# Kernel tuning notes

Measured on AMD Instinct MI355X. Metric: run time of the kernel, lower is better.

Reference implementation:

```python
import jax, jax.numpy as jnp
import numpy as np

# per-amino-acid residue lengths (heavy atoms - 1), 20 types, sorted ascending for readability
RES_LEN_NP = np.array([3, 4, 5, 5, 6, 6, 6, 7, 7, 7, 7, 7, 8, 8, 8, 9, 10, 10, 11, 13], dtype=np.int32)
LMAX = int(RES_LEN_NP.max())  # 13
N_TYPES = 20
N_RES = 2048
BATCH = 16
DV_ATM = 64
DV_AMN = 64


def _atoms_for(seq_types_np):
    return int(RES_LEN_NP[seq_types_np].sum())


def setup_inputs() -> dict:
    key = jax.random.key(0)
    k1, k2, k3, k4 = jax.random.split(key, 4)
    seq_np = (np.arange(N_RES) % N_TYPES).astype(np.int32)
    atoms = _atoms_for(seq_np)  # 15036
    pos_atm = jax.random.normal(k1, (BATCH, atoms, 3), dtype=jnp.float32)
    pos_amn = jax.random.normal(k2, (BATCH, N_RES, 3), dtype=jnp.float32)
    scale = 1.0 / np.sqrt(LMAX)
    W_amn = jax.random.normal(k3, (N_TYPES, DV_AMN, LMAX), dtype=jnp.float32) * scale
    W_atm = jax.random.normal(k4, (N_TYPES, LMAX, DV_ATM, LMAX), dtype=jnp.float32) * scale
    return {
        "pos_atm": pos_atm,
        "pos_amn": pos_amn,
        "W_amn": W_amn,
        "W_atm": W_atm,
        "seq_types": jnp.asarray(seq_np),
    }


def reference(pos_atm, pos_amn, W_amn, W_atm, seq_types):
    """Vectorized equivalent of the per-residue loop:
    for each residue i of type t with length L_t:
      diff = pos_atm[:, start_i:start_i+L_t] - pos_amn[:, i, None]        # (B, L_t, 3)
      x_v_amn[:, i] = einsum('ol,bld->bod', W_amn[t, :, :L_t], diff)       # (B, Damn, 3)
      x_v_atm block  = einsum('mvl,bld->bmvd', W_atm[t, :L_t, :, :L_t], diff)
    Residues are padded to LMAX and batched; padding is masked out.
    """
    res_len = jnp.asarray(RES_LEN_NP)
    B, atoms, _ = pos_atm.shape
    lens = res_len[seq_types]                                  # (N,)
    starts = jnp.concatenate([jnp.zeros((1,), lens.dtype), jnp.cumsum(lens)[:-1]])
    ar = jnp.arange(LMAX, dtype=lens.dtype)
    atom_idx = jnp.clip(starts[:, None] + ar[None, :], 0, atoms - 1)  # (N, LMAX)
    mask = ar[None, :] < lens[:, None]                                 # (N, LMAX)

    # diffs: (B, N, LMAX, 3), zeroed at padding
    diffs = (pos_atm[:, atom_idx] - pos_amn[:, :, None, :]) * mask[None, :, :, None]

    Wa = W_amn[seq_types]                                      # (N, Damn, LMAX)
    x_v_amn = jnp.einsum('bnld,nol->bnod', diffs, Wa)          # (B, N, Damn, 3)

    Wt = W_atm[seq_types]                                      # (N, LMAX, Dv, LMAX)
    xa = jnp.einsum('bnld,nmvl->bnmvd', diffs, Wt)             # (B, N, LMAX, Dv, 3)
    xa = xa * mask[None, :, :, None, None]

    # scatter padded per-residue atom outputs back to the flat atom axis;
    # invalid slots go to a dummy row `atoms` that is sliced off
    idx = jnp.where(mask, atom_idx, atoms).reshape(-1)         # (N*LMAX,)
    xa_flat = xa.reshape(B, -1, DV_ATM, 3)                     # (B, N*LMAX, Dv, 3)
    x_v_atm = jnp.zeros((B, atoms + 1, DV_ATM, 3), pos_atm.dtype).at[:, idx].add(xa_flat)[:, :atoms]
    return x_v_atm, x_v_amn
```

## Files before the change

### kernel.cpp

```cpp
#include <hip/hip_runtime.h>

#define N_RES 2048
#define BATCH 16
#define LMAX  13
#define NSLOT 14
#define VPAD  68
#define DV    64

__device__ __constant__ int RES_LEN_D[20] = {3,4,5,5,6,6,6,7,7,7,7,7,8,8,8,9,10,10,11,13};

__global__ __launch_bounds__(256, 3)
void posmix_kernel(const float* __restrict__ pos_atm,
                   const float* __restrict__ pos_amn,
                   const float* __restrict__ W_amn,
                   const float* __restrict__ W_atm,
                   const int*   __restrict__ seq,
                   float* __restrict__ out_atm,
                   float* __restrict__ out_amn,
                   int atoms)
{
  const int i   = blockIdx.x;
  const int tid = threadIdx.x;
  const int t   = seq[i];
  const int L   = RES_LEN_D[t];

  __shared__ float w_lds[NSLOT * LMAX * VPAD];
  __shared__ float diff_lds[BATCH * LMAX * 4];

  int* red = (int*)w_lds;
  {
    int s = 0;
    int base = tid * 8;
    #pragma unroll
    for (int k = 0; k < 8; ++k) {
      int r = base + k;
      if (r < i) s += RES_LEN_D[seq[r]];
    }
    red[tid] = s;
  }
  __syncthreads();
  #pragma unroll
  for (int off = 128; off > 0; off >>= 1) {
    if (tid < off) red[tid] += red[tid + off];
    __syncthreads();
  }
  const int start = red[0];
  __syncthreads();

  if (tid < BATCH * LMAX) {
    int b = tid / LMAX;
    int l = tid - b * LMAX;
    float dx = 0.f, dy = 0.f, dz = 0.f;
    if (l < L) {
      const float* pa = pos_atm + ((size_t)b * atoms + (size_t)(start + l)) * 3;
      const float* pm = pos_amn + ((size_t)b * N_RES + i) * 3;
      dx = pa[0] - pm[0];
      dy = pa[1] - pm[1];
      dz = pa[2] - pm[2];
    }
    *(float4*)(diff_lds + tid * 4) = make_float4(dx, dy, dz, 0.f);
  }

  {
    const float* Wt = W_atm + (size_t)t * (LMAX * DV * LMAX);
    const int total = L * DV * LMAX;
    for (int g = tid; g < total; g += 256) {
      int m = g / (DV * LMAX);
      int r = g - m * (DV * LMAX);
      int v = r / LMAX;
      int l = r - v * LMAX;
      w_lds[(m * LMAX + l) * VPAD + v] = Wt[g];
    }
    const float* Wa = W_amn + (size_t)t * (DV * LMAX);
    for (int g = tid; g < DV * LMAX; g += 256) {
      int o = g / LMAX;
      int l = g - o * LMAX;
      w_lds[(L * LMAX + l) * VPAD + o] = Wa[g];
    }
  }
  __syncthreads();

  const int Lp1 = L + 1;
  const int ntasks = 64 * Lp1;

  for (int task = tid; task < ntasks; task += 256) {
    int vo   = task & 7;
    int rest = task >> 3;
    int bp   = rest / Lp1;
    int m    = rest - bp * Lp1;

    float acc0[24], acc1[24];
    #pragma unroll
    for (int k = 0; k < 24; ++k) { acc0[k] = 0.f; acc1[k] = 0.f; }

    const float* wr = w_lds + (m * LMAX) * VPAD + vo * 8;
    const float* dr = diff_lds + (bp * 2) * (LMAX * 4);

    for (int l = 0; l < L; ++l) {
      float4 w0 = *(const float4*)(wr + l * VPAD);
      float4 w1 = *(const float4*)(wr + l * VPAD + 4);
      float4 d0 = *(const float4*)(dr + l * 4);
      float4 d1 = *(const float4*)(dr + (LMAX * 4) + l * 4);
      float wv[8] = {w0.x, w0.y, w0.z, w0.w, w1.x, w1.y, w1.z, w1.w};
      #pragma unroll
      for (int k = 0; k < 8; ++k) {
        acc0[k*3+0] += wv[k] * d0.x;
        acc0[k*3+1] += wv[k] * d0.y;
        acc0[k*3+2] += wv[k] * d0.z;
        acc1[k*3+0] += wv[k] * d1.x;
        acc1[k*3+1] += wv[k] * d1.y;
        acc1[k*3+2] += wv[k] * d1.z;
      }
    }

    const int b0 = bp * 2, b1 = b0 + 1;
    float* dst0;
    float* dst1;
    if (m < L) {
      size_t a = (size_t)(start + m);
      dst0 = out_atm + ((size_t)b0 * atoms + a) * (DV * 3) + vo * 24;
      dst1 = out_atm + ((size_t)b1 * atoms + a) * (DV * 3) + vo * 24;
    } else {
      dst0 = out_amn + ((size_t)b0 * N_RES + i) * (DV * 3) + vo * 24;
      dst1 = out_amn + ((size_t)b1 * N_RES + i) * (DV * 3) + vo * 24;
    }
    #pragma unroll
    for (int q = 0; q < 6; ++q) {
      ((float4*)dst0)[q] = make_float4(acc0[q*4+0], acc0[q*4+1], acc0[q*4+2], acc0[q*4+3]);
      ((float4*)dst1)[q] = make_float4(acc1[q*4+0], acc1[q*4+1], acc1[q*4+2], acc1[q*4+3]);
    }
  }
}

extern "C" void kernel_launch(void* const* d_in, const int* in_sizes, int n_in,
                              void* d_out, int out_size, void* d_ws, size_t ws_size,
                              hipStream_t stream) {
  const float* pos_atm = (const float*)d_in[0];
  const float* pos_amn = (const float*)d_in[1];
  const float* W_amn   = (const float*)d_in[2];
  const float* W_atm   = (const float*)d_in[3];
  const int*   seq     = (const int*)d_in[4];

  const int atoms = in_sizes[0] / (BATCH * 3);
  float* out_atm = (float*)d_out;
  float* out_amn = out_atm + (size_t)BATCH * atoms * DV * 3;

  posmix_kernel<<<N_RES, 256, 0, stream>>>(pos_atm, pos_amn, W_amn, W_atm, seq,
                                           out_atm, out_amn, atoms);
}
```

Baseline: 259.3 us.

## Remap compute tasks so lanes write contiguous float4 output chunks

Reorganizes the per-residue task decomposition. Each thread now computes a 4-float slice of the interleaved (v,d) output row for a 2x2 block of output rows and batches, instead of 24 contiguous floats for one row and two batches. Lanes in a wavefront therefore write adjacent float4s, making global stores coalesced. The diff buffer stores xyz twice per atom so a 4-wide window can straddle two v values. The weight padding is dropped. In exchange, threads have fewer accumulators and do more scalar LDS loads per FMA, and some LDS bank conflicts may appear.

```diff
diff --git a/kernel.cpp b/kernel.cpp
--- a/kernel.cpp
+++ b/kernel.cpp
@@ -4,8 +4,8 @@
 #define BATCH 16
 #define LMAX  13
 #define NSLOT 14
-#define VPAD  68
 #define DV    64
+#define DPAD  7
 
 __device__ __constant__ int RES_LEN_D[20] = {3,4,5,5,6,6,6,7,7,7,7,7,8,8,8,9,10,10,11,13};
 
@@ -23,9 +23,11 @@
   const int tid = threadIdx.x;
   const int t   = seq[i];
   const int L   = RES_LEN_D[t];
+  const int Lp1 = L + 1;
+  const int Mh  = (Lp1 + 1) >> 1;
 
-  __shared__ float w_lds[NSLOT * LMAX * VPAD];
-  __shared__ float diff_lds[BATCH * LMAX * 4];
+  __shared__ float w_lds[NSLOT * LMAX * DV];
+  __shared__ float diff_lds[BATCH * LMAX * DPAD];
 
   int* red = (int*)w_lds;
   {
@@ -58,7 +60,9 @@
       dy = pa[1] - pm[1];
       dz = pa[2] - pm[2];
     }
-    *(float4*)(diff_lds + tid * 4) = make_float4(dx, dy, dz, 0.f);
+    float* dd = diff_lds + tid * DPAD;
+    dd[0] = dx; dd[1] = dy; dd[2] = dz;
+    dd[3] = dx; dd[4] = dy; dd[5] = dz;
   }
 
   {
@@ -69,65 +73,76 @@
       int r = g - m * (DV * LMAX);
       int v = r / LMAX;
       int l = r - v * LMAX;
-      w_lds[(m * LMAX + l) * VPAD + v] = Wt[g];
+      w_lds[(m * LMAX + l) * DV + v] = Wt[g];
     }
     const float* Wa = W_amn + (size_t)t * (DV * LMAX);
     for (int g = tid; g < DV * LMAX; g += 256) {
       int o = g / LMAX;
       int l = g - o * LMAX;
-      w_lds[(L * LMAX + l) * VPAD + o] = Wa[g];
+      w_lds[(L * LMAX + l) * DV + o] = Wa[g];
     }
   }
   __syncthreads();
 
-  const int Lp1 = L + 1;
-  const int ntasks = 64 * Lp1;
+  const int ntasks = 48 * 8 * Mh;
 
   for (int task = tid; task < ntasks; task += 256) {
-    int vo   = task & 7;
-    int rest = task >> 3;
-    int bp   = rest / Lp1;
-    int m    = rest - bp * Lp1;
+    int lam = task % 48;
+    int rg  = task / 48;
+    int mh  = rg % Mh;
+    int bh  = rg / Mh;
+    int m0  = mh * 2, m1 = m0 + 1;
+    int b0  = bh * 2, b1 = b0 + 1;
 
-    float acc0[24], acc1[24];
-    #pragma unroll
-    for (int k = 0; k < 24; ++k) { acc0[k] = 0.f; acc1[k] = 0.f; }
+    int f0 = lam * 4;
+    int va = f0 / 3;
+    int r  = f0 - va * 3;
+    int th = 3 - r;
 
-    const float* wr = w_lds + (m * LMAX) * VPAD + vo * 8;
-    const float* dr = diff_lds + (bp * 2) * (LMAX * 4);
+    const float* w0 = w_lds + (m0 * LMAX) * DV + va;
+    const float* w1 = w_lds + (m1 * LMAX) * DV + va;
+    const float* p0 = diff_lds + (b0 * LMAX) * DPAD + r;
+    const float* p1 = diff_lds + (b1 * LMAX) * DPAD + r;
+
+    float a00[4] = {0.f,0.f,0.f,0.f};
+    float a01[4] = {0.f,0.f,0.f,0.f};
+    float a10[4] = {0.f,0.f,0.f,0.f};
+    float a11[4] = {0.f,0.f,0.f,0.f};
 
     for (int l = 0; l < L; ++l) {
-      float4 w0 = *(const float4*)(wr + l * VPAD);
-      float4 w1 = *(const float4*)(wr + l * VPAD + 4);
-      float4 d0 = *(const float4*)(dr + l * 4);
-      float4 d1 = *(const float4*)(dr + (LMAX * 4) + l * 4);
-      float wv[8] = {w0.x, w0.y, w0.z, w0.w, w1.x, w1.y, w1.z, w1.w};
+      float wa0 = w0[l * DV], wb0 = w0[l * DV + 1];
+      float wa1 = w1[l * DV], wb1 = w1[l * DV + 1];
+      float r0[4], r1[4];
       #pragma unroll
-      for (int k = 0; k < 8; ++k) {
-        acc0[k*3+0] += wv[k] * d0.x;
-        acc0[k*3+1] += wv[k] * d0.y;
-        acc0[k*3+2] += wv[k] * d0.z;
-        acc1[k*3+0] += wv[k] * d1.x;
-        acc1[k*3+1] += wv[k] * d1.y;
-        acc1[k*3+2] += wv[k] * d1.z;
+      for (int e = 0; e < 4; ++e) { r0[e] = p0[l * DPAD + e]; r1[e] = p1[l * DPAD + e]; }
+      #pragma unroll
+      for (int e = 0; e < 4; ++e) {
+        float ws0 = (e < th) ? wa0 : wb0;
+        float ws1 = (e < th) ? wa1 : wb1;
+        a00[e] += ws0 * r0[e];
+        a01[e] += ws0 * r1[e];
+        a10[e] += ws1 * r0[e];
+        a11[e] += ws1 * r1[e];
       }
     }
 
-    const int b0 = bp * 2, b1 = b0 + 1;
-    float* dst0;
-    float* dst1;
-    if (m < L) {
-      size_t a = (size_t)(start + m);
-      dst0 = out_atm + ((size_t)b0 * atoms + a) * (DV * 3) + vo * 24;
-      dst1 = out_atm + ((size_t)b1 * atoms + a) * (DV * 3) + vo * 24;
-    } else {
-      dst0 = out_amn + ((size_t)b0 * N_RES + i) * (DV * 3) + vo * 24;
-      dst1 = out_amn + ((size_t)b1 * N_RES + i) * (DV * 3) + vo * 24;
+    {
+      float* dst;
+      if (m0 < L) dst = out_atm + ((size_t)b0 * atoms + (size_t)(start + m0)) * 192 + f0;
+      else        dst = out_amn + ((size_t)b0 * N_RES + i) * 192 + f0;
+      *(float4*)dst = make_float4(a00[0], a00[1], a00[2], a00[3]);
+      if (m0 < L) dst = out_atm + ((size_t)b1 * atoms + (size_t)(start + m0)) * 192 + f0;
+      else        dst = out_amn + ((size_t)b1 * N_RES + i) * 192 + f0;
+      *(float4*)dst = make_float4(a01[0], a01[1], a01[2], a01[3]);
     }
-    #pragma unroll
-    for (int q = 0; q < 6; ++q) {
-      ((float4*)dst0)[q] = make_float4(acc0[q*4+0], acc0[q*4+1], acc0[q*4+2], acc0[q*4+3]);
-      ((float4*)dst1)[q] = make_float4(acc1[q*4+0], acc1[q*4+1], acc1[q*4+2], acc1[q*4+3]);
+    if (m1 <= L) {
+      float* dst;
+      if (m1 < L) dst = out_atm + ((size_t)b0 * atoms + (size_t)(start + m1)) * 192 + f0;
+      else        dst = out_amn + ((size_t)b0 * N_RES + i) * 192 + f0;
+      *(float4*)dst = make_float4(a10[0], a10[1], a10[2], a10[3]);
+      if (m1 < L) dst = out_atm + ((size_t)b1 * atoms + (size_t)(start + m1)) * 192 + f0;
+      else        dst = out_amn + ((size_t)b1 * N_RES + i) * 192 + f0;
+      *(float4*)dst = make_float4(a11[0], a11[1], a11[2], a11[3]);
     }
   }
 }
```

After: 245.6 us. 5.3% less time.
